# Optimization experiments

Measured on AMD Instinct MI355X. Metric: run time of the kernel, lower is better.

The kernel has to match this reference:

```python
import jax, jax.numpy as jnp
import numpy as np

N_NODES = 10000
N_EDGES = 640000
D_FEAT = 128
N_CLASSES = 40


def setup_inputs() -> dict:
    key = jax.random.key(0)
    k1, k2, k3, k4 = jax.random.split(key, 4)
    x = jax.random.normal(k1, (N_NODES, D_FEAT), dtype=jnp.float32)
    edge_index = jax.random.randint(k2, (2, N_EDGES), 0, N_NODES, dtype=jnp.int64)
    # SAGEConv params: lin_l (neighbor path, with bias), lin_r (root path, no bias)
    W_l = jax.random.normal(k3, (D_FEAT, N_CLASSES), dtype=jnp.float32) / np.sqrt(D_FEAT)
    b_l = jnp.zeros((N_CLASSES,), dtype=jnp.float32)
    W_r = jax.random.normal(k4, (D_FEAT, N_CLASSES), dtype=jnp.float32) / np.sqrt(D_FEAT)
    return {"x": x, "edge_index": edge_index, "W_l": W_l, "b_l": b_l, "W_r": W_r}


def reference(x, edge_index, W_l, b_l, W_r):
    # SAGEConv(aggr='max'): gather source features, scatter-max into destinations
    src, dst = edge_index[0], edge_index[1]
    msgs = x[src]                                        # [E, F] gather
    agg = jax.ops.segment_max(msgs, dst, num_segments=x.shape[0])  # [N, F]
    # nodes with no incoming edges: PyG fills with 0
    agg = jnp.where(jnp.isneginf(agg), 0.0, agg)
    out = agg @ W_l + b_l + x @ W_r                      # [N, C]
    return jax.nn.log_softmax(out, axis=1)
```

## Files before the change

### kernel.cpp

```cpp
#include <hip/hip_runtime.h>
#include <math.h>

#define D_FEAT 128
#define N_CLASSES 40
#define CAP 128
#define N_NODES_C 10000

#define CNT_PAD_INTS (N_NODES_C * 16)
#define XH_BYTES (N_NODES_C * D_FEAT * 2)
#define CNT_BYTES (CNT_PAD_INTS * 4)
#define WPK_U32 (64 * N_CLASSES)

typedef int v4i __attribute__((ext_vector_type(4)));
typedef _Float16 h2 __attribute__((ext_vector_type(2)));

static __device__ __forceinline__ unsigned int pkmax(unsigned int a, unsigned int b) {
    unsigned int d;
    asm("v_pk_max_f16 %0, %1, %2" : "=v"(d) : "v"(a), "v"(b));
    return d;
}
static __device__ __forceinline__ float fdot2(unsigned int a, unsigned int b, float c) {
    return __builtin_amdgcn_fdot2(__builtin_bit_cast(h2, a),
                                  __builtin_bit_cast(h2, b), c, false);
}
static __device__ __forceinline__ unsigned short f2h(float f) {
    return __builtin_bit_cast(unsigned short, (_Float16)f);
}


extern "C" __global__ void __launch_bounds__(256)
gnn_cvt(const float* __restrict__ x, unsigned int* __restrict__ xh,
        int* __restrict__ cnt,
        const float* __restrict__ W_l, const float* __restrict__ W_r,
        unsigned int* __restrict__ Wlpk, unsigned int* __restrict__ Wrpk, int n4)
{
    int t = blockIdx.x * 256 + threadIdx.x;
    if (t < CNT_PAD_INTS / 4) {
        reinterpret_cast<v4i*>(cnt)[t] = (v4i){0, 0, 0, 0};
    }
    if (t < WPK_U32) {
        int f2 = t / N_CLASSES, c = t % N_CLASSES;
        Wlpk[t] = (unsigned int)f2h(W_l[(2 * f2) * N_CLASSES + c])
                | ((unsigned int)f2h(W_l[(2 * f2 + 1) * N_CLASSES + c]) << 16);
        Wrpk[t] = (unsigned int)f2h(W_r[(2 * f2) * N_CLASSES + c])
                | ((unsigned int)f2h(W_r[(2 * f2 + 1) * N_CLASSES + c]) << 16);
    }
    if (t >= n4) return;
    float4 v = reinterpret_cast<const float4*>(x)[t];
    uint2 o;
    o.x = (unsigned int)f2h(v.x) | ((unsigned int)f2h(v.y) << 16);
    o.y = (unsigned int)f2h(v.z) | ((unsigned int)f2h(v.w) << 16);
    reinterpret_cast<uint2*>(xh)[t] = o;
}

extern "C" __global__ void __launch_bounds__(256)
gnn_bucketize(const int* __restrict__ src, const int* __restrict__ dst,
              int* __restrict__ cnt, unsigned short* __restrict__ bucket,
              int n_edges4)
{
    int t = blockIdx.x * 256 + threadIdx.x;
    if (t >= n_edges4) return;
    v4i s4 = __builtin_nontemporal_load(reinterpret_cast<const v4i*>(src) + t);
    v4i d4 = __builtin_nontemporal_load(reinterpret_cast<const v4i*>(dst) + t);
    int p0 = atomicAdd(&cnt[d4.x << 4], 1);
    int p1 = atomicAdd(&cnt[d4.y << 4], 1);
    int p2 = atomicAdd(&cnt[d4.z << 4], 1);
    int p3 = atomicAdd(&cnt[d4.w << 4], 1);
    if (p0 < CAP) bucket[(size_t)d4.x * CAP + p0] = (unsigned short)s4.x;
    if (p1 < CAP) bucket[(size_t)d4.y * CAP + p1] = (unsigned short)s4.y;
    if (p2 < CAP) bucket[(size_t)d4.z * CAP + p2] = (unsigned short)s4.z;
    if (p3 < CAP) bucket[(size_t)d4.w * CAP + p3] = (unsigned short)s4.w;
}

extern "C" __global__ void __launch_bounds__(256)
gnn_fused(const unsigned int* __restrict__ xh,
          const int* __restrict__ cnt, const unsigned short* __restrict__ bucket,
          const unsigned int* __restrict__ Wlpk, const unsigned int* __restrict__ Wrpk,
          const float* __restrict__ b_l,
          float* __restrict__ out, int n_nodes)
{
    __shared__ unsigned int sa2[4][64];
    __shared__ unsigned int sx2[4][64];

    const int wave = threadIdx.x >> 6;
    const int lane = threadIdx.x & 63;
    const int node = blockIdx.x * 4 + wave;
    const bool valid = (node < n_nodes);
    const int nclamp = min(node, n_nodes - 1);

    const int sub = lane >> 4;
    const int q   = lane & 15;

    const unsigned short* brow = bucket + (size_t)nclamp * CAP;
    const uint4* xh4 = reinterpret_cast<const uint4*>(xh);

    int id0 = brow[lane];
    int id1 = brow[64 + lane];
    uint4 xr;
    if (lane < 16) xr = xh4[nclamp * 16 + lane];
    float bias = (lane < N_CLASSES) ? b_l[lane] : 0.0f;
    int deg = valid ? min(cnt[nclamp << 4], CAP) : 0;

    unsigned int acc2[4];
    #pragma unroll
    for (int i = 0; i < 4; ++i) acc2[i] = 0xFC00FC00u;

    for (int base = 0; base < deg; base += 64) {
        const int nb = min(64, deg - base);
        const int myid = base ? id1 : id0;

        if (nb == 64) {
            #pragma unroll
            for (int k = 0; k < 64; k += 32) {
                int ss[8];
                #pragma unroll
                for (int j = 0; j < 8; ++j) ss[j] = __shfl(myid, k + 4 * j + sub, 64);
                uint4 vv[8];
                #pragma unroll
                for (int j = 0; j < 8; ++j) vv[j] = xh4[ss[j] * 16 + q];
                #pragma unroll
                for (int j = 0; j < 8; ++j) {
                    const unsigned int* u = &vv[j].x;
                    #pragma unroll
                    for (int w = 0; w < 4; ++w) acc2[w] = pkmax(acc2[w], u[w]);
                }
            }
        } else {
            for (int k = 0; k < nb; k += 8) {
                int e0 = min(k + sub, nb - 1);
                int e1 = min(k + 4 + sub, nb - 1);
                int s0 = __shfl(myid, e0, 64);
                int s1 = __shfl(myid, e1, 64);
                uint4 v0 = xh4[s0 * 16 + q];
                uint4 v1 = xh4[s1 * 16 + q];
                const unsigned int* u0 = &v0.x;
                const unsigned int* u1 = &v1.x;
                #pragma unroll
                for (int w = 0; w < 4; ++w) {
                    acc2[w] = pkmax(acc2[w], u0[w]);
                    acc2[w] = pkmax(acc2[w], u1[w]);
                }
            }
        }
    }

    #pragma unroll
    for (int i = 0; i < 4; ++i) {
        acc2[i] = pkmax(acc2[i], (unsigned int)__shfl_xor((int)acc2[i], 16, 64));
        acc2[i] = pkmax(acc2[i], (unsigned int)__shfl_xor((int)acc2[i], 32, 64));
    }
    if (deg == 0) {
        #pragma unroll
        for (int i = 0; i < 4; ++i) acc2[i] = 0u;
    }

    if (valid) {
        if (sub == 0) {
            uint4 w4;
            w4.x = acc2[0]; w4.y = acc2[1]; w4.z = acc2[2]; w4.w = acc2[3];
            *reinterpret_cast<uint4*>(&sa2[wave][q * 4]) = w4;
        }
        if (lane < 16) {
            reinterpret_cast<uint4*>(sx2[wave])[lane] = xr;
        }
    }

    float o = 0.0f;
    if (valid && lane < N_CLASSES) {
        o = bias;
        const uint4* a4 = reinterpret_cast<const uint4*>(sa2[wave]);
        const uint4* x4 = reinterpret_cast<const uint4*>(sx2[wave]);
        #pragma unroll 4
        for (int i = 0; i < 16; ++i) {
            uint4 a  = a4[i];
            uint4 xx = x4[i];
            const unsigned int* ua = &a.x;
            const unsigned int* ux = &xx.x;
            #pragma unroll
            for (int j = 0; j < 4; ++j) {
                int f2 = i * 4 + j;
                o = fdot2(ua[j], Wlpk[f2 * N_CLASSES + lane], o);
                o = fdot2(ux[j], Wrpk[f2 * N_CLASSES + lane], o);
            }
        }
    }

    float mm = (valid && lane < N_CLASSES) ? o : -INFINITY;
    #pragma unroll
    for (int off = 32; off > 0; off >>= 1) mm = fmaxf(mm, __shfl_xor(mm, off, 64));
    float ex = (valid && lane < N_CLASSES) ? expf(o - mm) : 0.0f;
    float ss = ex;
    #pragma unroll
    for (int off = 32; off > 0; off >>= 1) ss += __shfl_xor(ss, off, 64);

    if (valid && lane < N_CLASSES)
        out[(size_t)node * N_CLASSES + lane] = o - mm - logf(ss);
}

extern "C" void kernel_launch(void* const* d_in, const int* in_sizes, int n_in,
                              void* d_out, int out_size, void* d_ws, size_t ws_size,
                              hipStream_t stream) {
    const float* x   = (const float*)d_in[0];
    const int*   ei  = (const int*)d_in[1];
    const float* W_l = (const float*)d_in[2];
    const float* b_l = (const float*)d_in[3];
    const float* W_r = (const float*)d_in[4];
    float* out = (float*)d_out;

    const int n_nodes = in_sizes[0] / D_FEAT;
    const int n_edges = in_sizes[1] / 2;
    const int* src = ei;
    const int* dst = ei + n_edges;

    char* w = (char*)d_ws;
    unsigned int* xh = (unsigned int*)w;
    int* cnt = (int*)(w + XH_BYTES);
    unsigned int* Wlpk = (unsigned int*)(w + XH_BYTES + CNT_BYTES);
    unsigned int* Wrpk = Wlpk + WPK_U32;
    unsigned short* bucket = (unsigned short*)(w + XH_BYTES + CNT_BYTES
                                               + 2 * WPK_U32 * 4);

    {
        int n4 = n_nodes * D_FEAT / 4;
        int blocks = (n4 + 255) / 256;
        gnn_cvt<<<blocks, 256, 0, stream>>>(x, xh, cnt, W_l, W_r, Wlpk, Wrpk, n4);
    }
    {
        int n_edges4 = n_edges / 4;
        int blocks = (n_edges4 + 255) / 256;
        gnn_bucketize<<<blocks, 256, 0, stream>>>(src, dst, cnt, bucket, n_edges4);
    }
    {
        int blocks = (n_nodes + 3) / 4;
        gnn_fused<<<blocks, 256, 0, stream>>>(xh, cnt, bucket, Wlpk, Wrpk, b_l,
                                              out, n_nodes);
    }
}
```

Before: 60.52 us.

## Split each node's neighbor max-gather across two waves and merge via LDS

Each node's bucket of neighbors is now split in half, with each half gathered and max-reduced by its own wave. The two partial maxima are merged through shared memory after a block barrier, and only the first wave runs the dense projection and log-softmax. The separate remainder loop, which issued two loads per iteration, is replaced by the same 8-load unrolled loop with clamped neighbor indices. The aim is more memory-level parallelism and shorter per-node latency. The cost is a __syncthreads, redundant duplicate loads on partial chunks, and idle second waves during the matvec.

Result: slower. 61.93 us (+2.3%).

```diff
diff --git a/kernel.cpp b/kernel.cpp
--- a/kernel.cpp
+++ b/kernel.cpp
@@ -79,12 +79,14 @@
           const float* __restrict__ b_l,
           float* __restrict__ out, int n_nodes)
 {
-    __shared__ unsigned int sa2[4][64];
-    __shared__ unsigned int sx2[4][64];
+    __shared__ unsigned int sh2[4][64];
+    __shared__ unsigned int sx2[2][64];
 
     const int wave = threadIdx.x >> 6;
     const int lane = threadIdx.x & 63;
-    const int node = blockIdx.x * 4 + wave;
+    const int nloc = wave >> 1;
+    const int h    = wave & 1;
+    const int node = blockIdx.x * 2 + nloc;
     const bool valid = (node < n_nodes);
     const int nclamp = min(node, n_nodes - 1);
 
@@ -97,7 +99,7 @@
     int id0 = brow[lane];
     int id1 = brow[64 + lane];
     uint4 xr;
-    if (lane < 16) xr = xh4[nclamp * 16 + lane];
+    if (h == 0 && lane < 16) xr = xh4[nclamp * 16 + lane];
     float bias = (lane < N_CLASSES) ? b_l[lane] : 0.0f;
     int deg = valid ? min(cnt[nclamp << 4], CAP) : 0;
 
@@ -105,41 +107,29 @@
     #pragma unroll
     for (int i = 0; i < 4; ++i) acc2[i] = 0xFC00FC00u;
 
-    for (int base = 0; base < deg; base += 64) {
-        const int nb = min(64, deg - base);
-        const int myid = base ? id1 : id0;
-
-        if (nb == 64) {
-            #pragma unroll
-            for (int k = 0; k < 64; k += 32) {
-                int ss[8];
+    const int m = (deg + 1) >> 1;
+    const int ws = h ? m : 0;
+    const int we = h ? deg : m;
+
+    #pragma unroll 1
+    for (int part = 0; part < 2; ++part) {
+        const int base = part ? 64 : 0;
+        const int s0 = part ? max(ws, 64) : ws;
+        const int s1 = part ? we : min(we, 64);
+        for (int k = s0; k < s1; k += 32) {
+            const int myid = part ? id1 : id0;
+            int ss[8];
+            #pragma unroll
+            for (int j = 0; j < 8; ++j)
+                ss[j] = __shfl(myid, min(k + 4 * j + sub, s1 - 1) - base, 64);
+            uint4 vv[8];
+            #pragma unroll
+            for (int j = 0; j < 8; ++j) vv[j] = xh4[ss[j] * 16 + q];
+            #pragma unroll
+            for (int j = 0; j < 8; ++j) {
+                const unsigned int* u = &vv[j].x;
                 #pragma unroll
-                for (int j = 0; j < 8; ++j) ss[j] = __shfl(myid, k + 4 * j + sub, 64);
-                uint4 vv[8];
-                #pragma unroll
-                for (int j = 0; j < 8; ++j) vv[j] = xh4[ss[j] * 16 + q];
-                #pragma unroll
-                for (int j = 0; j < 8; ++j) {
-                    const unsigned int* u = &vv[j].x;
-                    #pragma unroll
-                    for (int w = 0; w < 4; ++w) acc2[w] = pkmax(acc2[w], u[w]);
-                }
-            }
-        } else {
-            for (int k = 0; k < nb; k += 8) {
-                int e0 = min(k + sub, nb - 1);
-                int e1 = min(k + 4 + sub, nb - 1);
-                int s0 = __shfl(myid, e0, 64);
-                int s1 = __shfl(myid, e1, 64);
-                uint4 v0 = xh4[s0 * 16 + q];
-                uint4 v1 = xh4[s1 * 16 + q];
-                const unsigned int* u0 = &v0.x;
-                const unsigned int* u1 = &v1.x;
-                #pragma unroll
-                for (int w = 0; w < 4; ++w) {
-                    acc2[w] = pkmax(acc2[w], u0[w]);
-                    acc2[w] = pkmax(acc2[w], u1[w]);
-                }
+                for (int w = 0; w < 4; ++w) acc2[w] = pkmax(acc2[w], u[w]);
             }
         }
     }
@@ -149,27 +139,34 @@
         acc2[i] = pkmax(acc2[i], (unsigned int)__shfl_xor((int)acc2[i], 16, 64));
         acc2[i] = pkmax(acc2[i], (unsigned int)__shfl_xor((int)acc2[i], 32, 64));
     }
-    if (deg == 0) {
-        #pragma unroll
-        for (int i = 0; i < 4; ++i) acc2[i] = 0u;
-    }
-
-    if (valid) {
-        if (sub == 0) {
-            uint4 w4;
-            w4.x = acc2[0]; w4.y = acc2[1]; w4.z = acc2[2]; w4.w = acc2[3];
-            *reinterpret_cast<uint4*>(&sa2[wave][q * 4]) = w4;
-        }
-        if (lane < 16) {
-            reinterpret_cast<uint4*>(sx2[wave])[lane] = xr;
-        }
+
+    if (sub == 0) {
+        uint4 w4;
+        w4.x = acc2[0]; w4.y = acc2[1]; w4.z = acc2[2]; w4.w = acc2[3];
+        *reinterpret_cast<uint4*>(&sh2[wave][q * 4]) = w4;
+    }
+    if (h == 0 && lane < 16) {
+        reinterpret_cast<uint4*>(sx2[nloc])[lane] = xr;
+    }
+    __syncthreads();
+
+    if (h == 1) return;
+
+    if (sub == 0) {
+        uint4 other = *reinterpret_cast<const uint4*>(&sh2[wave + 1][q * 4]);
+        uint4 w4;
+        w4.x = (deg == 0) ? 0u : pkmax(acc2[0], other.x);
+        w4.y = (deg == 0) ? 0u : pkmax(acc2[1], other.y);
+        w4.z = (deg == 0) ? 0u : pkmax(acc2[2], other.z);
+        w4.w = (deg == 0) ? 0u : pkmax(acc2[3], other.w);
+        *reinterpret_cast<uint4*>(&sh2[wave][q * 4]) = w4;
     }
 
     float o = 0.0f;
     if (valid && lane < N_CLASSES) {
         o = bias;
-        const uint4* a4 = reinterpret_cast<const uint4*>(sa2[wave]);
-        const uint4* x4 = reinterpret_cast<const uint4*>(sx2[wave]);
+        const uint4* a4 = reinterpret_cast<const uint4*>(sh2[wave]);
+        const uint4* x4 = reinterpret_cast<const uint4*>(sx2[nloc]);
         #pragma unroll 4
         for (int i = 0; i < 16; ++i) {
             uint4 a  = a4[i];
@@ -231,7 +228,7 @@
         gnn_bucketize<<<blocks, 256, 0, stream>>>(src, dst, cnt, bucket, n_edges4);
     }
     {
-        int blocks = (n_nodes + 3) / 4;
+        int blocks = (n_nodes + 1) / 2;
         gnn_fused<<<blocks, 256, 0, stream>>>(xh, cnt, bucket, Wlpk, Wrpk, b_l,
                                               out, n_nodes);
     }
```
